# Optimization experiments

Hardware: AMD Instinct MI355X
Metric: run time of the kernel (lower is better)

Reference implementation:

```python
import jax, jax.numpy as jnp
import numpy as np

H = 12          # num_attention_heads
D = 768         # hidden_size
DH = D // H     # attention_head_size
B, S = 8, 1024


def setup_inputs() -> dict:
    key = jax.random.key(0)
    ks = jax.random.split(key, 9)
    s_in = 1.0 / np.sqrt(D)
    x = jax.random.normal(ks[0], (B, S, D), dtype=jnp.float32)
    # per-head Q/K/V projections stacked over head axis: [H, D, DH]
    Wq = jax.random.uniform(ks[1], (H, D, DH), jnp.float32, -s_in, s_in)
    Wk = jax.random.uniform(ks[2], (H, D, DH), jnp.float32, -s_in, s_in)
    Wv = jax.random.uniform(ks[3], (H, D, DH), jnp.float32, -s_in, s_in)
    bq = jax.random.uniform(ks[4], (H, DH), jnp.float32, -s_in, s_in)
    bk = jax.random.uniform(ks[5], (H, DH), jnp.float32, -s_in, s_in)
    bv = jax.random.uniform(ks[6], (H, DH), jnp.float32, -s_in, s_in)
    s_out = 1.0 / np.sqrt(D)
    Wo = jax.random.uniform(ks[7], (D, D), jnp.float32, -s_out, s_out)
    bo = jax.random.uniform(ks[8], (D,), jnp.float32, -s_out, s_out)
    return {"x": x, "Wq": Wq, "bq": bq, "Wk": Wk, "bk": bk,
            "Wv": Wv, "bv": bv, "Wo": Wo, "bo": bo}


def reference(x, Wq, bq, Wk, bk, Wv, bv, Wo, bo):
    # batched per-head projections: [B,S,D] x [H,D,E] -> [B,H,S,E]
    q = jnp.einsum('bsd,hde->bhse', x, Wq) + bq[None, :, None, :]
    k = jnp.einsum('bsd,hde->bhse', x, Wk) + bk[None, :, None, :]
    v = jnp.einsum('bsd,hde->bhse', x, Wv) + bv[None, :, None, :]
    scores = jnp.einsum('bhse,bhte->bhst', q, k) / jnp.sqrt(
        jnp.asarray(DH, q.dtype))
    probs = jax.nn.softmax(scores, axis=-1)          # [B,H,S,S]
    ctx = jnp.einsum('bhst,bhte->bhse', probs, v)    # [B,H,S,E]
    # concat heads along last dim (head-major order, matching torch.cat)
    ctx = jnp.transpose(ctx, (0, 2, 1, 3)).reshape(B, S, H * DH)
    out = ctx @ Wo.T + bo
    return out, probs
```

## Files before the change

### kernel.cpp

```cpp
#include <hip/hip_runtime.h>
#include <cstddef>

#define Bn 8
#define Sn 1024
#define Hn 12
#define Dn 768
#define En 64
#define Mn (Bn * Sn)

typedef unsigned short ushort_t;
typedef __attribute__((ext_vector_type(4))) float f32x4;
typedef __bf16 bf16x8 __attribute__((ext_vector_type(8)));

#define MFMA(a, b, c) __builtin_amdgcn_mfma_f32_16x16x32_bf16(a, b, c, 0, 0, 0)

__device__ __forceinline__ ushort_t bf_hi(float f) {
    unsigned int u = __float_as_uint(f);
    return (ushort_t)((u + 0x7FFF + ((u >> 16) & 1)) >> 16);
}
__device__ __forceinline__ float bf_f(ushort_t s) {
    return __uint_as_float(((unsigned int)s) << 16);
}

#define GLL16(gp, lp)                                                        \
    __builtin_amdgcn_global_load_lds(                                        \
        (__attribute__((address_space(1))) void*)(gp),                       \
        (__attribute__((address_space(3))) void*)(lp), 16, 0, 0)

__global__ __launch_bounds__(256) void split_x_kernel(
    const float4* __restrict__ x4,
    ushort_t* __restrict__ xh, ushort_t* __restrict__ xl)
{
    int idx = blockIdx.x * 256 + threadIdx.x;
    float4 f = x4[idx];
    ushort_t h0 = bf_hi(f.x), h1 = bf_hi(f.y), h2 = bf_hi(f.z), h3 = bf_hi(f.w);
    ushort_t l0 = bf_hi(f.x - bf_f(h0));
    ushort_t l1 = bf_hi(f.y - bf_f(h1));
    ushort_t l2 = bf_hi(f.z - bf_f(h2));
    ushort_t l3 = bf_hi(f.w - bf_f(h3));
    *(ushort4*)&xh[(size_t)idx * 4] = make_ushort4(h0, h1, h2, h3);
    *(ushort4*)&xl[(size_t)idx * 4] = make_ushort4(l0, l1, l2, l3);
}

__global__ __launch_bounds__(256) void split_w_kernel(
    const float* __restrict__ Wq, const float* __restrict__ Wk,
    const float* __restrict__ Wv,
    ushort_t* __restrict__ wth, ushort_t* __restrict__ wtl)
{
    const int dt = blockIdx.x;
    const int h  = blockIdx.y;
    const int w  = blockIdx.z;
    const float* Wp = (w == 0) ? Wq : (w == 1) ? Wk : Wv;

    __shared__ float Ws[64][65];
    const int tid = threadIdx.x;

    #pragma unroll
    for (int t = 0; t < 16; ++t) {
        int idx = tid + t * 256;
        int d = idx >> 6, e = idx & 63;
        Ws[d][e] = Wp[((size_t)h * Dn + dt * 64 + d) * En + e];
    }
    __syncthreads();

    ushort_t* oh = wth + ((size_t)w * Hn + h) * En * Dn;
    ushort_t* ol = wtl + ((size_t)w * Hn + h) * En * Dn;
    #pragma unroll
    for (int t = 0; t < 16; ++t) {
        int idx = tid + t * 256;
        int e = idx >> 6, dd = idx & 63;
        float f = Ws[dd][e];
        ushort_t hi = bf_hi(f);
        oh[(size_t)e * Dn + dt * 64 + dd] = hi;
        ol[(size_t)e * Dn + dt * 64 + dd] = bf_hi(f - bf_f(hi));
    }
}

__global__ __launch_bounds__(256) void qkv_mfma_kernel(
    const ushort_t* __restrict__ xh, const ushort_t* __restrict__ xl,
    const ushort_t* __restrict__ wth, const ushort_t* __restrict__ wtl,
    const float* __restrict__ bq, const float* __restrict__ bk,
    const float* __restrict__ bv,
    ushort_t* __restrict__ Qh, ushort_t* __restrict__ Ql,
    ushort_t* __restrict__ Kh, ushort_t* __restrict__ Kl,
    ushort_t* __restrict__ Vth, ushort_t* __restrict__ Vtl)
{
    const int mt = blockIdx.x;
    const int h  = blockIdx.y;
    const int w  = blockIdx.z;
    const float* bp = (w == 0) ? bq : (w == 1) ? bk : bv;
    ushort_t* OH = (w == 0) ? Qh : (w == 1) ? Kh : Vth;
    ushort_t* OL = (w == 0) ? Ql : (w == 1) ? Kl : Vtl;
    const ushort_t* Wh = wth + ((size_t)w * Hn + h) * En * Dn;
    const ushort_t* Wl = wtl + ((size_t)w * Hn + h) * En * Dn;

    __shared__ __align__(16) ushort_t Ah[128 * 64];
    __shared__ __align__(16) ushort_t Al[128 * 64];
    __shared__ __align__(16) ushort_t Bh[64 * 64];
    __shared__ __align__(16) ushort_t Bl[64 * 64];

    const int tid  = threadIdx.x;
    const int lane = tid & 63;
    const int lr   = lane & 15, lg = lane >> 4;
    const int wid  = tid >> 6;
    const int wm   = wid >> 1;
    const int wn   = wid & 1;
    const int m0   = mt * 128;

    f32x4 acc[4][2] = {};

    for (int k0 = 0; k0 < Dn; k0 += 64) {
        if (k0) __syncthreads();
        #pragma unroll
        for (int t = 0; t < 4; ++t) {
            int c = tid + t * 256;
            int r = c >> 3, sl = (c & 7) ^ (r & 7);
            size_t go = (size_t)(m0 + r) * Dn + k0 + sl * 8;
            GLL16(xh + go, &Ah[c * 8]);
            GLL16(xl + go, &Al[c * 8]);
        }
        #pragma unroll
        for (int t = 0; t < 2; ++t) {
            int c = tid + t * 256;
            int r = c >> 3, sl = (c & 7) ^ (r & 7);
            size_t go = (size_t)r * Dn + k0 + sl * 8;
            GLL16(Wh + go, &Bh[c * 8]);
            GLL16(Wl + go, &Bl[c * 8]);
        }
        __syncthreads();

        #pragma unroll
        for (int ks = 0; ks < 2; ++ks) {
            const int kb = ks * 32 + lg * 8;
            bf16x8 a_h[4], a_l[4], b_h[2], b_l[2];
            #pragma unroll
            for (int i = 0; i < 4; ++i) {
                int row = wm * 64 + i * 16 + lr;
                int ai = (row * 64 + kb) ^ ((row & 7) << 3);
                a_h[i] = *(const bf16x8*)&Ah[ai];
                a_l[i] = *(const bf16x8*)&Al[ai];
            }
            #pragma unroll
            for (int j = 0; j < 2; ++j) {
                int col = wn * 32 + j * 16 + lr;
                int bi = (col * 64 + kb) ^ ((col & 7) << 3);
                b_h[j] = *(const bf16x8*)&Bh[bi];
                b_l[j] = *(const bf16x8*)&Bl[bi];
            }
            #pragma unroll
            for (int i = 0; i < 4; ++i)
                #pragma unroll
                for (int j = 0; j < 2; ++j) {
                    acc[i][j] = MFMA(a_h[i], b_h[j], acc[i][j]);
                    acc[i][j] = MFMA(a_l[i], b_h[j], acc[i][j]);
                    acc[i][j] = MFMA(a_h[i], b_l[j], acc[i][j]);
                }
        }
    }

    #pragma unroll
    for (int j = 0; j < 2; ++j) {
        int col = wn * 32 + j * 16 + lr;
        float bb = bp[h * En + col];
        #pragma unroll
        for (int i = 0; i < 4; ++i) {
            #pragma unroll
            for (int r = 0; r < 4; ++r) {
                int m = m0 + wm * 64 + i * 16 + lg * 4 + r;
                int bidx = m >> 10, s = m & 1023;
                float v = acc[i][j][r] + bb;
                ushort_t vh = bf_hi(v);
                ushort_t vl = bf_hi(v - bf_f(vh));
                size_t off;
                if (w < 2)
                    off = (size_t)((bidx * Hn + h) * Sn + s) * En + col;
                else
                    off = (size_t)((bidx * Hn + h) * En + col) * Sn + s;
                OH[off] = vh;
                OL[off] = vl;
            }
        }
    }
}

__global__ __launch_bounds__(256) void attn_kernel(
    const ushort_t* __restrict__ Qh, const ushort_t* __restrict__ Ql,
    const ushort_t* __restrict__ Kh_g, const ushort_t* __restrict__ Kl_g,
    const ushort_t* __restrict__ Vth_g, const ushort_t* __restrict__ Vtl_g,
    float* __restrict__ Pr,
    ushort_t* __restrict__ CTXh, ushort_t* __restrict__ CTXl)
{
    const int qt = blockIdx.x;
    const int bh = blockIdx.y;
    const int bb = bh / Hn, h = bh % Hn;

    __shared__ __align__(16) ushort_t Ks[2][64 * 64];
    __shared__ __align__(16) ushort_t Vs[2][64 * 64];
    __shared__ __align__(16) ushort_t Ps[2][64 * 64];

    const int tid = threadIdx.x, lane = tid & 63, w = tid >> 6;
    const int lr = lane & 15, lg = lane >> 4;

    const ushort_t* KH  = Kh_g  + (size_t)bh * Sn * En;
    const ushort_t* KL  = Kl_g  + (size_t)bh * Sn * En;
    const ushort_t* VTH = Vth_g + (size_t)bh * En * Sn;
    const ushort_t* VTL = Vtl_g + (size_t)bh * En * Sn;

    bf16x8 qfh[2], qfl[2];
    {
        size_t off = ((size_t)bh * Sn + qt * 64 + w * 16 + lr) * En + lg * 8;
        qfh[0] = *(const bf16x8*)&Qh[off];
        qfh[1] = *(const bf16x8*)&Qh[off + 32];
        qfl[0] = *(const bf16x8*)&Ql[off];
        qfl[1] = *(const bf16x8*)&Ql[off + 32];
    }

    float rs[4] = {0.f, 0.f, 0.f, 0.f};

    for (int kt = 0; kt < 16; ++kt) {
        __syncthreads();
        #pragma unroll
        for (int t = 0; t < 2; ++t) {
            int c = tid + t * 256;
            int r = c >> 3, sl = (c & 7) ^ (r & 7);
            size_t go = (size_t)(kt * 64 + r) * En + sl * 8;
            GLL16(KH + go, &Ks[0][c * 8]);
            GLL16(KL + go, &Ks[1][c * 8]);
        }
        __syncthreads();

        f32x4 sacc[4] = {};
        #pragma unroll
        for (int ks = 0; ks < 2; ++ks) {
            #pragma unroll
            for (int j = 0; j < 4; ++j) {
                int key = j * 16 + lr;
                int bi = (key * 64 + ks * 32 + lg * 8) ^ ((key & 7) << 3);
                bf16x8 kh = *(const bf16x8*)&Ks[0][bi];
                bf16x8 kl = *(const bf16x8*)&Ks[1][bi];
                sacc[j] = MFMA(qfh[ks], kh, sacc[j]);
                sacc[j] = MFMA(qfl[ks], kh, sacc[j]);
                sacc[j] = MFMA(qfh[ks], kl, sacc[j]);
            }
        }
        #pragma unroll
        for (int j = 0; j < 4; ++j)
            #pragma unroll
            for (int r = 0; r < 4; ++r)
                rs[r] += __expf(0.125f * sacc[j][r]);
    }
    #pragma unroll
    for (int r = 0; r < 4; ++r) {
        float v = rs[r];
        v += __shfl_xor(v, 1);
        v += __shfl_xor(v, 2);
        v += __shfl_xor(v, 4);
        v += __shfl_xor(v, 8);
        rs[r] = 1.f / v;
    }

    f32x4 cacc[4] = {};
    float* PrRow = Pr + ((size_t)bh * Sn + qt * 64) * Sn;

    for (int kt = 0; kt < 16; ++kt) {
        __syncthreads();
        #pragma unroll
        for (int t = 0; t < 2; ++t) {
            int c = tid + t * 256;
            int r = c >> 3, sl = (c & 7) ^ (r & 7);
            size_t gk = (size_t)(kt * 64 + r) * En + sl * 8;
            GLL16(KH + gk, &Ks[0][c * 8]);
            GLL16(KL + gk, &Ks[1][c * 8]);
            size_t gv = (size_t)r * Sn + kt * 64 + sl * 8;
            GLL16(VTH + gv, &Vs[0][c * 8]);
            GLL16(VTL + gv, &Vs[1][c * 8]);
        }
        __syncthreads();

        f32x4 sacc[4] = {};
        #pragma unroll
        for (int ks = 0; ks < 2; ++ks) {
            #pragma unroll
            for (int j = 0; j < 4; ++j) {
                int key = j * 16 + lr;
                int bi = (key * 64 + ks * 32 + lg * 8) ^ ((key & 7) << 3);
                bf16x8 kh = *(const bf16x8*)&Ks[0][bi];
                bf16x8 kl = *(const bf16x8*)&Ks[1][bi];
                sacc[j] = MFMA(qfh[ks], kh, sacc[j]);
                sacc[j] = MFMA(qfl[ks], kh, sacc[j]);
                sacc[j] = MFMA(qfh[ks], kl, sacc[j]);
            }
        }

        #pragma unroll
        for (int j = 0; j < 4; ++j) {
            int key = j * 16 + lr;
            #pragma unroll
            for (int r = 0; r < 4; ++r) {
                int q = w * 16 + lg * 4 + r;
                float p = __expf(0.125f * sacc[j][r]) * rs[r];
                PrRow[(size_t)q * Sn + kt * 64 + key] = p;
                ushort_t ph = bf_hi(p);
                int pi = (q * 64 + key) ^ ((q & 7) << 3);
                Ps[0][pi] = ph;
                Ps[1][pi] = bf_hi(p - bf_f(ph));
            }
        }

        #pragma unroll
        for (int ks = 0; ks < 2; ++ks) {
            int qa = w * 16 + lr;
            int ai = (qa * 64 + ks * 32 + lg * 8) ^ ((qa & 7) << 3);
            bf16x8 pah = *(const bf16x8*)&Ps[0][ai];
            bf16x8 pal = *(const bf16x8*)&Ps[1][ai];
            #pragma unroll
            for (int j = 0; j < 4; ++j) {
                int er = j * 16 + lr;
                int bi = (er * 64 + ks * 32 + lg * 8) ^ ((er & 7) << 3);
                bf16x8 vh = *(const bf16x8*)&Vs[0][bi];
                bf16x8 vl = *(const bf16x8*)&Vs[1][bi];
                cacc[j] = MFMA(pah, vh, cacc[j]);
                cacc[j] = MFMA(pal, vh, cacc[j]);
                cacc[j] = MFMA(pah, vl, cacc[j]);
            }
        }
    }

    #pragma unroll
    for (int j = 0; j < 4; ++j) {
        #pragma unroll
        for (int r = 0; r < 4; ++r) {
            int s = qt * 64 + w * 16 + lg * 4 + r;
            int e = j * 16 + lr;
            float v = cacc[j][r];
            ushort_t vh = bf_hi(v);
            size_t off = ((size_t)bb * Sn + s) * Dn + h * En + e;
            CTXh[off] = vh;
            CTXl[off] = bf_hi(v - bf_f(vh));
        }
    }
}

__global__ __launch_bounds__(256) void out_mfma_kernel(
    const ushort_t* __restrict__ CTXh, const ushort_t* __restrict__ CTXl,
    const float* __restrict__ Wo, const float* __restrict__ bo,
    float* __restrict__ out)
{
    const int mt = blockIdx.x;
    const int nt = blockIdx.y;

    __shared__ __align__(16) ushort_t Ah[128 * 64];
    __shared__ __align__(16) ushort_t Al[128 * 64];
    __shared__ __align__(16) ushort_t Bh[64 * 64];
    __shared__ __align__(16) ushort_t Bl[64 * 64];

    const int tid  = threadIdx.x;
    const int lane = tid & 63;
    const int lr   = lane & 15, lg = lane >> 4;
    const int wid  = tid >> 6;
    const int wm   = wid >> 1, wn = wid & 1;
    const int m0   = mt * 128, n0 = nt * 64;

    f32x4 acc[4][2] = {};

    for (int k0 = 0; k0 < Dn; k0 += 64) {
        if (k0) __syncthreads();
        #pragma unroll
        for (int t = 0; t < 4; ++t) {
            int c = tid + t * 256;
            int r = c >> 3, sl = (c & 7) ^ (r & 7);
            size_t go = (size_t)(m0 + r) * Dn + k0 + sl * 8;
            GLL16(CTXh + go, &Ah[c * 8]);
            GLL16(CTXl + go, &Al[c * 8]);
        }
        #pragma unroll
        for (int t = 0; t < 4; ++t) {
            int idx = tid + t * 256;
            int n = idx >> 4, f4 = idx & 15;
            float4 f = *(const float4*)&Wo[(size_t)(n0 + n) * Dn + k0 + f4 * 4];
            ushort_t h0 = bf_hi(f.x), h1 = bf_hi(f.y);
            ushort_t h2 = bf_hi(f.z), h3 = bf_hi(f.w);
            unsigned int hi0 = (unsigned)h0 | ((unsigned)h1 << 16);
            unsigned int hi1 = (unsigned)h2 | ((unsigned)h3 << 16);
            unsigned int lo0 = (unsigned)bf_hi(f.x - bf_f(h0)) |
                               ((unsigned)bf_hi(f.y - bf_f(h1)) << 16);
            unsigned int lo1 = (unsigned)bf_hi(f.z - bf_f(h2)) |
                               ((unsigned)bf_hi(f.w - bf_f(h3)) << 16);
            int di = (n * 64 + f4 * 4) ^ ((n & 7) << 3);
            *(uint2*)&Bh[di] = make_uint2(hi0, hi1);
            *(uint2*)&Bl[di] = make_uint2(lo0, lo1);
        }
        __syncthreads();

        #pragma unroll
        for (int ks = 0; ks < 2; ++ks) {
            const int kb = ks * 32 + lg * 8;
            bf16x8 a_h[4], a_l[4], b_h[2], b_l[2];
            #pragma unroll
            for (int i = 0; i < 4; ++i) {
                int row = wm * 64 + i * 16 + lr;
                int ai = (row * 64 + kb) ^ ((row & 7) << 3);
                a_h[i] = *(const bf16x8*)&Ah[ai];
                a_l[i] = *(const bf16x8*)&Al[ai];
            }
            #pragma unroll
            for (int j = 0; j < 2; ++j) {
                int col = wn * 32 + j * 16 + lr;
                int bi = (col * 64 + kb) ^ ((col & 7) << 3);
                b_h[j] = *(const bf16x8*)&Bh[bi];
                b_l[j] = *(const bf16x8*)&Bl[bi];
            }
            #pragma unroll
            for (int i = 0; i < 4; ++i)
                #pragma unroll
                for (int j = 0; j < 2; ++j) {
                    acc[i][j] = MFMA(a_h[i], b_h[j], acc[i][j]);
                    acc[i][j] = MFMA(a_l[i], b_h[j], acc[i][j]);
                    acc[i][j] = MFMA(a_h[i], b_l[j], acc[i][j]);
                }
        }
    }

    #pragma unroll
    for (int j = 0; j < 2; ++j) {
        int col = n0 + wn * 32 + j * 16 + lr;
        float bb = bo[col];
        #pragma unroll
        for (int i = 0; i < 4; ++i)
            #pragma unroll
            for (int r = 0; r < 4; ++r) {
                int m = m0 + wm * 64 + i * 16 + lg * 4 + r;
                out[(size_t)m * Dn + col] = acc[i][j][r] + bb;
            }
    }
}

extern "C" void kernel_launch(void* const* d_in, const int* in_sizes, int n_in,
                              void* d_out, int out_size, void* d_ws, size_t ws_size,
                              hipStream_t stream)
{
    const float* x  = (const float*)d_in[0];
    const float* Wq = (const float*)d_in[1];
    const float* bq = (const float*)d_in[2];
    const float* Wk = (const float*)d_in[3];
    const float* bk = (const float*)d_in[4];
    const float* Wv = (const float*)d_in[5];
    const float* bv = (const float*)d_in[6];
    const float* Wo = (const float*)d_in[7];
    const float* bo = (const float*)d_in[8];

    float* out = (float*)d_out;
    const size_t QSZ = (size_t)Bn * Hn * Sn * En;
    float* probs = out + (size_t)Bn * Sn * Dn;

    ushort_t* u   = (ushort_t*)d_ws;
    ushort_t* Qh  = u;
    ushort_t* Ql  = Qh + QSZ;
    ushort_t* Kh  = Ql + QSZ;
    ushort_t* Kl  = Kh + QSZ;
    ushort_t* Vth = Kl + QSZ;
    ushort_t* Vtl = Vth + QSZ;
    ushort_t* xh  = Vtl + QSZ;
    ushort_t* xl  = xh + (size_t)Mn * Dn;
    ushort_t* CTXh = xh;
    ushort_t* CTXl = xl;

    ushort_t* wth = (ushort_t*)probs;
    ushort_t* wtl = wth + (size_t)3 * Hn * En * Dn;

    split_x_kernel<<<dim3(Mn * Dn / 4 / 256), 256, 0, stream>>>(
        (const float4*)x, xh, xl);

    split_w_kernel<<<dim3(Dn / 64, Hn, 3), 256, 0, stream>>>(
        Wq, Wk, Wv, wth, wtl);

    qkv_mfma_kernel<<<dim3(Mn / 128, Hn, 3), 256, 0, stream>>>(
        xh, xl, wth, wtl, bq, bk, bv, Qh, Ql, Kh, Kl, Vth, Vtl);

    attn_kernel<<<dim3(Sn / 64, Bn * Hn), 256, 0, stream>>>(
        Qh, Ql, Kh, Kl, Vth, Vtl, probs, CTXh, CTXl);

    out_mfma_kernel<<<dim3(Mn / 128, Dn / 64), 256, 0, stream>>>(
        CTXh, CTXl, Wo, bo, out);
}
```

Measured before the change: 742.9 us.

## Retile attention to 128-query blocks with 32x32 MFMA and single-term P

The attention kernel now processes 128 queries per block (32 per wave) using 32x32x16 bf16 MFMAs, which doubles K/V reuse per LDS load and halves the grid. The row-sum pass loads 128 keys per iteration, and P@V now uses only the high bf16 part of P (two MFMAs instead of three), which drops the low-part P store and its matmul work. Context output is written as vectorized ushort4 stores, and launch bounds request 3 blocks per CU. The cost is lower precision in the context (P is truncated to bf16) and higher register pressure from the 16-wide accumulators.

```diff
diff --git a/kernel.cpp b/kernel.cpp
--- a/kernel.cpp
+++ b/kernel.cpp
@@ -10,9 +10,11 @@
 
 typedef unsigned short ushort_t;
 typedef __attribute__((ext_vector_type(4))) float f32x4;
+typedef __attribute__((ext_vector_type(16))) float f32x16;
 typedef __bf16 bf16x8 __attribute__((ext_vector_type(8)));
 
-#define MFMA(a, b, c) __builtin_amdgcn_mfma_f32_16x16x32_bf16(a, b, c, 0, 0, 0)
+#define MFMA(a, b, c)   __builtin_amdgcn_mfma_f32_16x16x32_bf16(a, b, c, 0, 0, 0)
+#define MFMA32(a, b, c) __builtin_amdgcn_mfma_f32_32x32x16_bf16(a, b, c, 0, 0, 0)
 
 __device__ __forceinline__ ushort_t bf_hi(float f) {
     unsigned int u = __float_as_uint(f);
@@ -183,7 +185,7 @@
     }
 }
 
-__global__ __launch_bounds__(256) void attn_kernel(
+__global__ __launch_bounds__(256, 3) void attn_kernel(
     const ushort_t* __restrict__ Qh, const ushort_t* __restrict__ Ql,
     const ushort_t* __restrict__ Kh_g, const ushort_t* __restrict__ Kl_g,
     const ushort_t* __restrict__ Vth_g, const ushort_t* __restrict__ Vtl_g,
@@ -194,73 +196,79 @@
     const int bh = blockIdx.y;
     const int bb = bh / Hn, h = bh % Hn;
 
-    __shared__ __align__(16) ushort_t Ks[2][64 * 64];
-    __shared__ __align__(16) ushort_t Vs[2][64 * 64];
-    __shared__ __align__(16) ushort_t Ps[2][64 * 64];
+    __shared__ __align__(16) ushort_t KV[4][64 * 64];
+    __shared__ __align__(16) ushort_t Ps[128 * 64];
 
     const int tid = threadIdx.x, lane = tid & 63, w = tid >> 6;
-    const int lr = lane & 15, lg = lane >> 4;
+    const int l31 = lane & 31, lh = lane >> 5;
 
     const ushort_t* KH  = Kh_g  + (size_t)bh * Sn * En;
     const ushort_t* KL  = Kl_g  + (size_t)bh * Sn * En;
     const ushort_t* VTH = Vth_g + (size_t)bh * En * Sn;
     const ushort_t* VTL = Vtl_g + (size_t)bh * En * Sn;
 
-    bf16x8 qfh[2], qfl[2];
+    bf16x8 qh[4], ql[4];
     {
-        size_t off = ((size_t)bh * Sn + qt * 64 + w * 16 + lr) * En + lg * 8;
-        qfh[0] = *(const bf16x8*)&Qh[off];
-        qfh[1] = *(const bf16x8*)&Qh[off + 32];
-        qfl[0] = *(const bf16x8*)&Ql[off];
-        qfl[1] = *(const bf16x8*)&Ql[off + 32];
-    }
-
-    float rs[4] = {0.f, 0.f, 0.f, 0.f};
-
-    for (int kt = 0; kt < 16; ++kt) {
+        size_t off = ((size_t)bh * Sn + qt * 128 + w * 32 + l31) * En + lh * 8;
+        #pragma unroll
+        for (int kc = 0; kc < 4; ++kc) {
+            qh[kc] = *(const bf16x8*)&Qh[off + kc * 16];
+            ql[kc] = *(const bf16x8*)&Ql[off + kc * 16];
+        }
+    }
+
+    float rs[16];
+    #pragma unroll
+    for (int i = 0; i < 16; ++i) rs[i] = 0.f;
+
+    for (int kr = 0; kr < 8; ++kr) {
         __syncthreads();
         #pragma unroll
         for (int t = 0; t < 2; ++t) {
             int c = tid + t * 256;
             int r = c >> 3, sl = (c & 7) ^ (r & 7);
-            size_t go = (size_t)(kt * 64 + r) * En + sl * 8;
-            GLL16(KH + go, &Ks[0][c * 8]);
-            GLL16(KL + go, &Ks[1][c * 8]);
-        }
-        __syncthreads();
-
-        f32x4 sacc[4] = {};
-        #pragma unroll
-        for (int ks = 0; ks < 2; ++ks) {
-            #pragma unroll
-            for (int j = 0; j < 4; ++j) {
-                int key = j * 16 + lr;
-                int bi = (key * 64 + ks * 32 + lg * 8) ^ ((key & 7) << 3);
-                bf16x8 kh = *(const bf16x8*)&Ks[0][bi];
-                bf16x8 kl = *(const bf16x8*)&Ks[1][bi];
-                sacc[j] = MFMA(qfh[ks], kh, sacc[j]);
-                sacc[j] = MFMA(qfl[ks], kh, sacc[j]);
-                sacc[j] = MFMA(qfh[ks], kl, sacc[j]);
-            }
-        }
-        #pragma unroll
-        for (int j = 0; j < 4; ++j)
-            #pragma unroll
-            for (int r = 0; r < 4; ++r)
-                rs[r] += __expf(0.125f * sacc[j][r]);
-    }
-    #pragma unroll
-    for (int r = 0; r < 4; ++r) {
-        float v = rs[r];
+            size_t g0 = (size_t)(kr * 128 + r) * En + sl * 8;
+            size_t g1 = (size_t)(kr * 128 + 64 + r) * En + sl * 8;
+            GLL16(KH + g0, &KV[0][c * 8]);
+            GLL16(KL + g0, &KV[1][c * 8]);
+            GLL16(KH + g1, &KV[2][c * 8]);
+            GLL16(KL + g1, &KV[3][c * 8]);
+        }
+        __syncthreads();
+
+        #pragma unroll
+        for (int kt = 0; kt < 4; ++kt) {
+            const ushort_t* bhp = KV[(kt >> 1) * 2];
+            const ushort_t* blp = KV[(kt >> 1) * 2 + 1];
+            int krow = (kt & 1) * 32 + l31;
+            f32x16 sacc = {};
+            #pragma unroll
+            for (int kc = 0; kc < 4; ++kc) {
+                int bi = (krow * 64 + kc * 16 + lh * 8) ^ ((krow & 7) << 3);
+                bf16x8 kh = *(const bf16x8*)&bhp[bi];
+                bf16x8 kl = *(const bf16x8*)&blp[bi];
+                sacc = MFMA32(qh[kc], kh, sacc);
+                sacc = MFMA32(ql[kc], kh, sacc);
+                sacc = MFMA32(qh[kc], kl, sacc);
+            }
+            #pragma unroll
+            for (int rg = 0; rg < 16; ++rg)
+                rs[rg] += __expf(0.125f * sacc[rg]);
+        }
+    }
+    #pragma unroll
+    for (int rg = 0; rg < 16; ++rg) {
+        float v = rs[rg];
         v += __shfl_xor(v, 1);
         v += __shfl_xor(v, 2);
         v += __shfl_xor(v, 4);
         v += __shfl_xor(v, 8);
-        rs[r] = 1.f / v;
-    }
-
-    f32x4 cacc[4] = {};
-    float* PrRow = Pr + ((size_t)bh * Sn + qt * 64) * Sn;
+        v += __shfl_xor(v, 16);
+        rs[rg] = 1.f / v;
+    }
+
+    f32x16 cacc[2] = {};
+    float* PrB = Pr + ((size_t)bh * Sn + qt * 128 + w * 32) * Sn;
 
     for (int kt = 0; kt < 16; ++kt) {
         __syncthreads();
@@ -269,74 +277,75 @@
             int c = tid + t * 256;
             int r = c >> 3, sl = (c & 7) ^ (r & 7);
             size_t gk = (size_t)(kt * 64 + r) * En + sl * 8;
-            GLL16(KH + gk, &Ks[0][c * 8]);
-            GLL16(KL + gk, &Ks[1][c * 8]);
             size_t gv = (size_t)r * Sn + kt * 64 + sl * 8;
-            GLL16(VTH + gv, &Vs[0][c * 8]);
-            GLL16(VTL + gv, &Vs[1][c * 8]);
-        }
-        __syncthreads();
-
-        f32x4 sacc[4] = {};
-        #pragma unroll
-        for (int ks = 0; ks < 2; ++ks) {
-            #pragma unroll
-            for (int j = 0; j < 4; ++j) {
-                int key = j * 16 + lr;
-                int bi = (key * 64 + ks * 32 + lg * 8) ^ ((key & 7) << 3);
-                bf16x8 kh = *(const bf16x8*)&Ks[0][bi];
-                bf16x8 kl = *(const bf16x8*)&Ks[1][bi];
-                sacc[j] = MFMA(qfh[ks], kh, sacc[j]);
-                sacc[j] = MFMA(qfl[ks], kh, sacc[j]);
-                sacc[j] = MFMA(qfh[ks], kl, sacc[j]);
-            }
-        }
-
-        #pragma unroll
-        for (int j = 0; j < 4; ++j) {
-            int key = j * 16 + lr;
-            #pragma unroll
-            for (int r = 0; r < 4; ++r) {
-                int q = w * 16 + lg * 4 + r;
-                float p = __expf(0.125f * sacc[j][r]) * rs[r];
-                PrRow[(size_t)q * Sn + kt * 64 + key] = p;
-                ushort_t ph = bf_hi(p);
-                int pi = (q * 64 + key) ^ ((q & 7) << 3);
-                Ps[0][pi] = ph;
-                Ps[1][pi] = bf_hi(p - bf_f(ph));
-            }
-        }
-
-        #pragma unroll
-        for (int ks = 0; ks < 2; ++ks) {
-            int qa = w * 16 + lr;
-            int ai = (qa * 64 + ks * 32 + lg * 8) ^ ((qa & 7) << 3);
-            bf16x8 pah = *(const bf16x8*)&Ps[0][ai];
-            bf16x8 pal = *(const bf16x8*)&Ps[1][ai];
-            #pragma unroll
-            for (int j = 0; j < 4; ++j) {
-                int er = j * 16 + lr;
-                int bi = (er * 64 + ks * 32 + lg * 8) ^ ((er & 7) << 3);
-                bf16x8 vh = *(const bf16x8*)&Vs[0][bi];
-                bf16x8 vl = *(const bf16x8*)&Vs[1][bi];
-                cacc[j] = MFMA(pah, vh, cacc[j]);
-                cacc[j] = MFMA(pal, vh, cacc[j]);
-                cacc[j] = MFMA(pah, vl, cacc[j]);
-            }
-        }
-    }
-
-    #pragma unroll
-    for (int j = 0; j < 4; ++j) {
-        #pragma unroll
-        for (int r = 0; r < 4; ++r) {
-            int s = qt * 64 + w * 16 + lg * 4 + r;
-            int e = j * 16 + lr;
-            float v = cacc[j][r];
-            ushort_t vh = bf_hi(v);
-            size_t off = ((size_t)bb * Sn + s) * Dn + h * En + e;
-            CTXh[off] = vh;
-            CTXl[off] = bf_hi(v - bf_f(vh));
+            GLL16(KH + gk, &KV[0][c * 8]);
+            GLL16(KL + gk, &KV[1][c * 8]);
+            GLL16(VTH + gv, &KV[2][c * 8]);
+            GLL16(VTL + gv, &KV[3][c * 8]);
+        }
+        __syncthreads();
+
+        #pragma unroll
+        for (int ktile = 0; ktile < 2; ++ktile) {
+            int krow = ktile * 32 + l31;
+            f32x16 sacc = {};
+            #pragma unroll
+            for (int kc = 0; kc < 4; ++kc) {
+                int bi = (krow * 64 + kc * 16 + lh * 8) ^ ((krow & 7) << 3);
+                bf16x8 kh = *(const bf16x8*)&KV[0][bi];
+                bf16x8 kl = *(const bf16x8*)&KV[1][bi];
+                sacc = MFMA32(qh[kc], kh, sacc);
+                sacc = MFMA32(ql[kc], kh, sacc);
+                sacc = MFMA32(qh[kc], kl, sacc);
+            }
+            #pragma unroll
+            for (int rg = 0; rg < 16; ++rg) {
+                int qloc = (rg & 3) + 8 * (rg >> 2) + 4 * lh;
+                float p = __expf(0.125f * sacc[rg]) * rs[rg];
+                PrB[(size_t)qloc * Sn + kt * 64 + ktile * 32 + l31] = p;
+                int pi = ((w * 32 + qloc) * 64 + ktile * 32 + l31)
+                         ^ ((qloc & 7) << 3);
+                Ps[pi] = bf_hi(p);
+            }
+        }
+
+        #pragma unroll
+        for (int kc = 0; kc < 4; ++kc) {
+            int bi2 = ((w * 32 + l31) * 64 + kc * 16 + lh * 8)
+                      ^ ((l31 & 7) << 3);
+            bf16x8 pb = *(const bf16x8*)&Ps[bi2];
+            #pragma unroll
+            for (int et = 0; et < 2; ++et) {
+                int vrow = et * 32 + l31;
+                int ai = (vrow * 64 + kc * 16 + lh * 8) ^ ((vrow & 7) << 3);
+                bf16x8 vh = *(const bf16x8*)&KV[2][ai];
+                bf16x8 vl = *(const bf16x8*)&KV[3][ai];
+                cacc[et] = MFMA32(vh, pb, cacc[et]);
+                cacc[et] = MFMA32(vl, pb, cacc[et]);
+            }
+        }
+    }
+
+    {
+        int s = qt * 128 + w * 32 + l31;
+        size_t base = ((size_t)bb * Sn + s) * Dn + h * En;
+        #pragma unroll
+        for (int et = 0; et < 2; ++et) {
+            #pragma unroll
+            for (int rg = 0; rg < 4; ++rg) {
+                int e0 = et * 32 + rg * 8 + 4 * lh;
+                ushort_t hv[4], lv[4];
+                #pragma unroll
+                for (int i = 0; i < 4; ++i) {
+                    float v = cacc[et][rg * 4 + i];
+                    hv[i] = bf_hi(v);
+                    lv[i] = bf_hi(v - bf_f(hv[i]));
+                }
+                *(ushort4*)&CTXh[base + e0] =
+                    make_ushort4(hv[0], hv[1], hv[2], hv[3]);
+                *(ushort4*)&CTXl[base + e0] =
+                    make_ushort4(lv[0], lv[1], lv[2], lv[3]);
+            }
         }
     }
 }
@@ -477,7 +486,7 @@
     qkv_mfma_kernel<<<dim3(Mn / 128, Hn, 3), 256, 0, stream>>>(
         xh, xl, wth, wtl, bq, bk, bv, Qh, Ql, Kh, Kl, Vth, Vtl);
 
-    attn_kernel<<<dim3(Sn / 64, Bn * Hn), 256, 0, stream>>>(
+    attn_kernel<<<dim3(Sn / 128, Bn * Hn), 256, 0, stream>>>(
         Qh, Ql, Kh, Kl, Vth, Vtl, probs, CTXh, CTXl);
 
     out_mfma_kernel<<<dim3(Mn / 128, Dn / 64), 256, 0, stream>>>(
```

Measured after the change: 826.6 us. +11.3%, slower.
